# Optimization experiments

Measured on AMD Instinct MI355X. Metric: run time of the kernel, lower is better.

Reference implementation:

```python
import jax, jax.numpy as jnp
import numpy as np
from jax import lax

# Module constraint: hidden_dim == state_dim == expand_dim (see broadcasting in original).
H = 128  # hidden_dim
N = 128  # state_dim
E = 128  # expand_dim = hidden_dim * expand_factor (expand_factor=1)
B, L = 4, 1024


def setup_inputs() -> dict:
    key = jax.random.key(0)
    ks = jax.random.split(key, 11)
    s = lambda fan: 1.0 / np.sqrt(fan)
    return {
        "u": jax.random.normal(ks[0], (B, L, H), jnp.float32),
        "W_in": jax.random.normal(ks[1], (H, 2 * E), jnp.float32) * s(H),
        "b_in": jax.random.normal(ks[2], (2 * E,), jnp.float32) * 0.01,
        "conv_w": jax.random.normal(ks[3], (E, 1, 3), jnp.float32) * s(3),
        "conv_b": jax.random.normal(ks[4], (E,), jnp.float32) * 0.01,
        "W_x": jax.random.normal(ks[5], (E, N + N + H), jnp.float32) * s(E),
        "b_x": jax.random.normal(ks[6], (N + N + H,), jnp.float32) * 0.01,
        "A_log": jax.random.normal(ks[7], (N,), jnp.float32),
        "D": jnp.ones((H,), jnp.float32),
        "W_out": jax.random.normal(ks[8], (E, H), jnp.float32) * s(E),
        "b_out": jax.random.normal(ks[9], (H,), jnp.float32) * 0.01,
    }


def reference(u, W_in, b_in, conv_w, conv_b, W_x, b_x, A_log, D, W_out, b_out):
    b, l, _ = u.shape
    xz = u @ W_in + b_in                       # [B,L,2E]
    x, z = jnp.split(xz, 2, axis=-1)           # [B,L,E] each
    # depthwise conv1d, kernel 3, padding 1 (groups == channels)
    xc = lax.conv_general_dilated(
        x.transpose(0, 2, 1), conv_w, window_strides=(1,), padding=[(1, 1)],
        feature_group_count=E, dimension_numbers=("NCH", "OIH", "NCH"))
    x = jax.nn.silu(xc.transpose(0, 2, 1) + conv_b)  # [B,L,E]
    ssm = x @ W_x + b_x                        # [B,L,2N+H]
    delta = jax.nn.softplus(ssm[..., :N])      # [B,L,N]
    Bm = ssm[..., N:2 * N]                     # [B,L,N]
    C = ssm[..., 2 * N:]                       # [B,L,H]
    A = -jnp.exp(A_log)                        # [N]

    def step(h, inp):
        d_t, B_t, C_t, x_t, u_t = inp          # [B,N],[B,N],[B,H],[B,E],[B,H]
        # A_discrete[b,t,i,j] = exp(delta[b,t,i] * A[j])  (outer broadcast, as in source)
        A_disc = jnp.exp(d_t[:, :, None] * A[None, None, :])       # [B,N,N]
        h = A_disc * h + (d_t * B_t)[:, :, None] * x_t[:, None, :]  # [B,N,E]
        y = (h * C_t[:, None, :]).sum(axis=1) + D * u_t             # [B,H]
        return h, y

    h0 = jnp.zeros((b, N, H), u.dtype)
    inputs = (delta.transpose(1, 0, 2), Bm.transpose(1, 0, 2),
              C.transpose(1, 0, 2), x.transpose(1, 0, 2), u.transpose(1, 0, 2))
    _, ys = lax.scan(step, h0, inputs)         # ys: [L,B,H]
    y = ys.transpose(1, 0, 2) * jax.nn.silu(z)  # [B,L,H] (E==H)
    return y @ W_out + b_out                   # dropout in eval mode: identity
```

## Files before the change

kernel.cpp:

```cpp
#include <hip/hip_runtime.h>
#include <hip/hip_bf16.h>

using bf16 = __hip_bfloat16;
typedef __attribute__((ext_vector_type(8))) short short8;
typedef __attribute__((ext_vector_type(4))) float f32x4;

#define BVAL 4
#define LVAL 1024
#define LOG2E 1.44269504f

#define TSEG 64
#define SSEG 16
#define RSTR 144

#define OFF_U      0
#define OFF_WIN    524288
#define OFF_BIN    557056
#define OFF_CONVW  557312
#define OFF_CONVB  557696
#define OFF_WX     557824
#define OFF_BX     606976
#define OFF_ALOG   607360
#define OFF_D      607488
#define OFF_WOUT   607616
#define OFF_BOUT   624000
#define CVT_TOTAL  624128

#define CVT2_U   524288
#define CVT2_WI  (CVT2_U + 32768)
#define CVT2_WX  (CVT2_WI + 49152)
#define CVT2_TOT (CVT2_WX + 16384)

__device__ __forceinline__ int dtype_flag(const void* D) {
    return ((*(const unsigned int*)D) & 0xFFFFu) != 0u ? 1 : 0;
}
__device__ __forceinline__ float ldin(const void* p, int i, int f) {
    return f ? __bfloat162float(((const bf16*)p)[i]) : ((const float*)p)[i];
}

__global__ void kcvt_all(const void* __restrict__ u, const void* __restrict__ W_in,
                         const void* __restrict__ b_in, const void* __restrict__ conv_w,
                         const void* __restrict__ conv_b, const void* __restrict__ W_x,
                         const void* __restrict__ b_x, const void* __restrict__ A_log,
                         const void* __restrict__ D, const void* __restrict__ W_out,
                         const void* __restrict__ b_out, float* __restrict__ dst,
                         bf16* __restrict__ ubf, bf16* __restrict__ wtin,
                         bf16* __restrict__ wtx, bf16* __restrict__ wtout) {
    int idx = blockIdx.x * 256 + threadIdx.x;
    int f = dtype_flag(D);
    if (idx < CVT_TOTAL) {
        const void* p; int loc;
        if      (idx < OFF_WIN)   { p = u;      loc = idx; }
        else if (idx < OFF_BIN)   { p = W_in;   loc = idx - OFF_WIN; }
        else if (idx < OFF_CONVW) { p = b_in;   loc = idx - OFF_BIN; }
        else if (idx < OFF_CONVB) { p = conv_w; loc = idx - OFF_CONVW; }
        else if (idx < OFF_WX)    { p = conv_b; loc = idx - OFF_CONVB; }
        else if (idx < OFF_BX)    { p = W_x;    loc = idx - OFF_WX; }
        else if (idx < OFF_ALOG)  { p = b_x;    loc = idx - OFF_BX; }
        else if (idx < OFF_D)     { p = A_log;  loc = idx - OFF_ALOG; }
        else if (idx < OFF_WOUT)  { p = D;      loc = idx - OFF_D; }
        else if (idx < OFF_BOUT)  { p = W_out;  loc = idx - OFF_WOUT; }
        else                      { p = b_out;  loc = idx - OFF_BOUT; }
        dst[idx] = ldin(p, loc, f);
    } else {
        int ix = idx - CVT_TOTAL;
        if (ix >= CVT2_TOT) return;
        if (ix < CVT2_U) {
            ubf[ix] = __float2bfloat16(ldin(u, ix, f));
        } else if (ix < CVT2_WI) {
            int rel = ix - CVT2_U; int n = rel >> 7, k = rel & 127;
            wtin[rel] = __float2bfloat16(ldin(W_in, k * 256 + n, f));
        } else if (ix < CVT2_WX) {
            int rel = ix - CVT2_WI; int n = rel >> 7, k = rel & 127;
            wtx[rel] = __float2bfloat16(ldin(W_x, k * 384 + n, f));
        } else {
            int rel = ix - CVT2_WX; int n = rel >> 7, k = rel & 127;
            wtout[rel] = __float2bfloat16(ldin(W_out, k * 128 + n, f));
        }
    }
}

__global__ void k1_mfma(const bf16* __restrict__ ubf, const bf16* __restrict__ wtin,
                        const float* __restrict__ cvt,
                        float* __restrict__ x_pre, float* __restrict__ zs) {
    int blk = blockIdx.x, mb = blk >> 3, cb = blk & 7;
    int tid = threadIdx.x, w = tid >> 6, lane = tid & 63;
    int quad = lane >> 4, sub = lane & 15;
    int m0 = mb * 64 + w * 16, c = cb * 16;
    f32x4 accX = {0.f, 0.f, 0.f, 0.f}, accZ = {0.f, 0.f, 0.f, 0.f};
    #pragma unroll
    for (int ks = 0; ks < 4; ++ks) {
        int k0 = ks * 32 + quad * 8;
        short8 a  = *(const short8*)(ubf + (size_t)(m0 + sub) * 128 + k0);
        short8 bX = *(const short8*)(wtin + (size_t)(c + sub) * 128 + k0);
        short8 bZ = *(const short8*)(wtin + (size_t)(128 + c + sub) * 128 + k0);
        accX = __builtin_amdgcn_mfma_f32_16x16x32_bf16(a, bX, accX, 0, 0, 0);
        accZ = __builtin_amdgcn_mfma_f32_16x16x32_bf16(a, bZ, accZ, 0, 0, 0);
    }
    int o = c + sub;
    float bx_ = cvt[OFF_BIN + o], bz_ = cvt[OFF_BIN + 128 + o];
    #pragma unroll
    for (int r = 0; r < 4; ++r) {
        int m = m0 + quad * 4 + r;
        float x = accX[r] + bx_;
        float z = accZ[r] + bz_;
        x_pre[(size_t)m * 128 + o] = x;
        zs[(size_t)m * 128 + o] = z / (1.0f + __expf(-z));
    }
}

__global__ void k2_conv(const float* __restrict__ cvt, const float* __restrict__ x_pre,
                        float* __restrict__ xs, bf16* __restrict__ xsbf) {
    const float* conv_w = cvt + OFF_CONVW;
    const float* conv_b = cvt + OFF_CONVB;
    int q = blockIdx.x * 256 + threadIdx.x;
    int basee = q * 4;
    int row = basee >> 7;
    int l = row & (LVAL - 1);
    int e = basee & 127;
    float4 xc = *(const float4*)(x_pre + basee);
    float4 xm = make_float4(0.f, 0.f, 0.f, 0.f);
    float4 xp = make_float4(0.f, 0.f, 0.f, 0.f);
    if (l > 0)        xm = *(const float4*)(x_pre + basee - 128);
    if (l < LVAL - 1) xp = *(const float4*)(x_pre + basee + 128);
    float mm[4] = {xm.x, xm.y, xm.z, xm.w};
    float cc[4] = {xc.x, xc.y, xc.z, xc.w};
    float pp[4] = {xp.x, xp.y, xp.z, xp.w};
    float out[4];
    #pragma unroll
    for (int i = 0; i < 4; ++i) {
        float w0 = conv_w[(e + i) * 3 + 0];
        float w1 = conv_w[(e + i) * 3 + 1];
        float w2 = conv_w[(e + i) * 3 + 2];
        float v = fmaf(w0, mm[i], fmaf(w1, cc[i], fmaf(w2, pp[i], conv_b[e + i])));
        out[i] = v / (1.0f + __expf(-v));
    }
    *(float4*)(xs + basee) = make_float4(out[0], out[1], out[2], out[3]);
    #pragma unroll
    for (int i = 0; i < 4; ++i) xsbf[basee + i] = __float2bfloat16(out[i]);
}

__global__ void k3_mfma(const bf16* __restrict__ xsbf, const bf16* __restrict__ wtx,
                        const float* __restrict__ cvt,
                        float* __restrict__ delta, float* __restrict__ dB,
                        float* __restrict__ Cc) {
    int blk = blockIdx.x, mb = blk >> 3, cb = blk & 7;
    int tid = threadIdx.x, w = tid >> 6, lane = tid & 63;
    int quad = lane >> 4, sub = lane & 15;
    int m0 = mb * 64 + w * 16, c = cb * 16;
    f32x4 accA = {0.f,0.f,0.f,0.f}, accB = {0.f,0.f,0.f,0.f}, accC = {0.f,0.f,0.f,0.f};
    #pragma unroll
    for (int ks = 0; ks < 4; ++ks) {
        int k0 = ks * 32 + quad * 8;
        short8 a  = *(const short8*)(xsbf + (size_t)(m0 + sub) * 128 + k0);
        short8 bA = *(const short8*)(wtx + (size_t)(c + sub) * 128 + k0);
        short8 bB = *(const short8*)(wtx + (size_t)(128 + c + sub) * 128 + k0);
        short8 bC = *(const short8*)(wtx + (size_t)(256 + c + sub) * 128 + k0);
        accA = __builtin_amdgcn_mfma_f32_16x16x32_bf16(a, bA, accA, 0, 0, 0);
        accB = __builtin_amdgcn_mfma_f32_16x16x32_bf16(a, bB, accB, 0, 0, 0);
        accC = __builtin_amdgcn_mfma_f32_16x16x32_bf16(a, bC, accC, 0, 0, 0);
    }
    int o = c + sub;
    float ba = cvt[OFF_BX + o], bb = cvt[OFF_BX + 128 + o], bc = cvt[OFF_BX + 256 + o];
    #pragma unroll
    for (int r = 0; r < 4; ++r) {
        int m = m0 + quad * 4 + r;
        size_t idx = (size_t)m * 128 + o;
        float d = accA[r] + ba;
        float sp = (d > 20.0f) ? d : log1pf(__expf(d));
        delta[idx] = sp;
        dB[idx] = sp * (accB[r] + bb);
        Cc[idx] = accC[r] + bc;
    }
}

__device__ __forceinline__ void stage_chunk(float* sdl, float* swl, int tid,
                                            const float4 rd[2], const float4 rw[2]) {
    #pragma unroll
    for (int i = 0; i < 2; ++i) {
        int q = i * 256 + tid;
        int t = q >> 5, n4 = q & 31, l = n4 >> 1, hf = n4 & 1;
        int ad = t * RSTR + 8 * l + 4 * (l >> 2) + 4 * hf;
        *(float4*)&sdl[ad] = rd[i];
        *(float4*)&swl[ad] = rw[i];
    }
}

__global__ __launch_bounds__(256, 2)
void k5a(const float* __restrict__ cvt, const float* __restrict__ delta,
         const float* __restrict__ dB, const float* __restrict__ xs,
         float* __restrict__ hout, float* __restrict__ Pout) {
    __shared__ float sdl[2][16 * RSTR], swl[2][16 * RSTR];
    __shared__ float sx[TSEG][16];
    int blk = blockIdx.x;
    int b = blk >> 7, s = (blk >> 3) & 15, jg = blk & 7;
    int tid = threadIdx.x, w = tid >> 6, lane = tid & 63;
    int cj = lane >> 4, ln = lane & 15;
    int jj = w * 4 + cj, j = jg * 16 + jj;
    int t0 = s * TSEG;
    size_t base = (size_t)b * (LVAL * 128);
    {
        int t = tid >> 2, jc = tid & 3;
        *(float4*)&sx[t][jc * 4] =
            *(const float4*)(xs + base + (size_t)(t0 + t) * 128 + jg * 16 + jc * 4);
    }
    float a2 = -__expf(cvt[OFF_ALOG + j]) * LOG2E;
    const float4* gd4 = (const float4*)(delta + base);
    const float4* gw4 = (const float4*)(dB + base);
    float h[8], p[8];
    #pragma unroll
    for (int i = 0; i < 8; ++i) { h[i] = 0.f; p[i] = 1.f; }
    int fb = t0 * 32;
    float4 rd[2], rw[2];
    rd[0] = gd4[fb + tid]; rd[1] = gd4[fb + 256 + tid];
    rw[0] = gw4[fb + tid]; rw[1] = gw4[fb + 256 + tid];
    stage_chunk(sdl[0], swl[0], tid, rd, rw);
    __syncthreads();
    for (int c4 = 0; c4 < 4; ++c4) {
        if (c4 < 3) {
            int f2 = fb + (c4 + 1) * 512;
            rd[0] = gd4[f2 + tid]; rd[1] = gd4[f2 + 256 + tid];
            rw[0] = gw4[f2 + tid]; rw[1] = gw4[f2 + 256 + tid];
        }
        int bf = c4 & 1;
        int rbase = 8 * ln + 4 * (ln >> 2);
        #pragma unroll 4
        for (int k = 0; k < 16; ++k) {
            int bl = k * RSTR + rbase;
            float4 d0 = *(const float4*)&sdl[bf][bl];
            float4 d1 = *(const float4*)&sdl[bf][bl + 4];
            float4 w0 = *(const float4*)&swl[bf][bl];
            float4 w1 = *(const float4*)&swl[bf][bl + 4];
            float xv = sx[c4 * 16 + k][jj];
            float e;
            e = exp2f(d0.x * a2); h[0] = fmaf(e, h[0], w0.x * xv); p[0] *= e;
            e = exp2f(d0.y * a2); h[1] = fmaf(e, h[1], w0.y * xv); p[1] *= e;
            e = exp2f(d0.z * a2); h[2] = fmaf(e, h[2], w0.z * xv); p[2] *= e;
            e = exp2f(d0.w * a2); h[3] = fmaf(e, h[3], w0.w * xv); p[3] *= e;
            e = exp2f(d1.x * a2); h[4] = fmaf(e, h[4], w1.x * xv); p[4] *= e;
            e = exp2f(d1.y * a2); h[5] = fmaf(e, h[5], w1.y * xv); p[5] *= e;
            e = exp2f(d1.z * a2); h[6] = fmaf(e, h[6], w1.z * xv); p[6] *= e;
            e = exp2f(d1.w * a2); h[7] = fmaf(e, h[7], w1.w * xv); p[7] *= e;
        }
        if (c4 < 3) stage_chunk(sdl[(c4 + 1) & 1], swl[(c4 + 1) & 1], tid, rd, rw);
        __syncthreads();
    }
    size_t cb = (((size_t)(b * SSEG + s) * 128 + j) * 128) + 8 * ln;
    *(float4*)(hout + cb)     = make_float4(h[0], h[1], h[2], h[3]);
    *(float4*)(hout + cb + 4) = make_float4(h[4], h[5], h[6], h[7]);
    *(float4*)(Pout + cb)     = make_float4(p[0], p[1], p[2], p[3]);
    *(float4*)(Pout + cb + 4) = make_float4(p[4], p[5], p[6], p[7]);
}

__global__ __launch_bounds__(256, 2)
void k5c(const float* __restrict__ cvt, const float* __restrict__ delta,
         const float* __restrict__ dB, const float* __restrict__ Cc,
         const float* __restrict__ xs, const float* __restrict__ zs,
         const float* __restrict__ hout, const float* __restrict__ Pout,
         bf16* __restrict__ y2bf) {
    __shared__ float sdl[2][16 * RSTR], swl[2][16 * RSTR];
    __shared__ float sx[TSEG][16], sc[TSEG][16], su[TSEG][16], sz[TSEG][16];
    int blk = blockIdx.x;
    int b = blk >> 7, s = (blk >> 3) & 15, jg = blk & 7;
    int tid = threadIdx.x, w = tid >> 6, lane = tid & 63;
    int cj = lane >> 4, ln = lane & 15;
    int jj = w * 4 + cj, j = jg * 16 + jj;
    int t0 = s * TSEG;
    size_t base = (size_t)b * (LVAL * 128);
    {
        int t = tid >> 2, jc = tid & 3;
        size_t g = base + (size_t)(t0 + t) * 128 + jg * 16 + jc * 4;
        *(float4*)&sx[t][jc * 4] = *(const float4*)(xs + g);
        *(float4*)&sc[t][jc * 4] = *(const float4*)(Cc + g);
        *(float4*)&su[t][jc * 4] = *(const float4*)(cvt + OFF_U + g);
        *(float4*)&sz[t][jc * 4] = *(const float4*)(zs + g);
    }
    float a2 = -__expf(cvt[OFF_ALOG + j]) * LOG2E;
    float Dj = cvt[OFF_D + j];
    const float4* gd4 = (const float4*)(delta + base);
    const float4* gw4 = (const float4*)(dB + base);
    int fb = t0 * 32;
    float4 rd[2], rw[2];
    rd[0] = gd4[fb + tid]; rd[1] = gd4[fb + 256 + tid];
    rw[0] = gw4[fb + tid]; rw[1] = gw4[fb + 256 + tid];
    float h[8];
    #pragma unroll
    for (int i = 0; i < 8; ++i) h[i] = 0.f;
    size_t cstep = (size_t)128 * 128;
    size_t cb0 = (((size_t)(b * SSEG) * 128 + j) * 128) + 8 * ln;
    for (int sp = 0; sp < s; ++sp) {
        size_t cb = cb0 + (size_t)sp * cstep;
        float4 ho0 = *(const float4*)(hout + cb);
        float4 ho1 = *(const float4*)(hout + cb + 4);
        float4 pp0 = *(const float4*)(Pout + cb);
        float4 pp1 = *(const float4*)(Pout + cb + 4);
        h[0] = fmaf(pp0.x, h[0], ho0.x); h[1] = fmaf(pp0.y, h[1], ho0.y);
        h[2] = fmaf(pp0.z, h[2], ho0.z); h[3] = fmaf(pp0.w, h[3], ho0.w);
        h[4] = fmaf(pp1.x, h[4], ho1.x); h[5] = fmaf(pp1.y, h[5], ho1.y);
        h[6] = fmaf(pp1.z, h[6], ho1.z); h[7] = fmaf(pp1.w, h[7], ho1.w);
    }
    stage_chunk(sdl[0], swl[0], tid, rd, rw);
    __syncthreads();
    for (int c4 = 0; c4 < 4; ++c4) {
        if (c4 < 3) {
            int f2 = fb + (c4 + 1) * 512;
            rd[0] = gd4[f2 + tid]; rd[1] = gd4[f2 + 256 + tid];
            rw[0] = gw4[f2 + tid]; rw[1] = gw4[f2 + 256 + tid];
        }
        int bf = c4 & 1;
        int rbase = 8 * ln + 4 * (ln >> 2);
        #pragma unroll 4
        for (int k = 0; k < 16; ++k) {
            int bl = k * RSTR + rbase;
            float4 d0 = *(const float4*)&sdl[bf][bl];
            float4 d1 = *(const float4*)&sdl[bf][bl + 4];
            float4 w0 = *(const float4*)&swl[bf][bl];
            float4 w1 = *(const float4*)&swl[bf][bl + 4];
            int t = c4 * 16 + k;
            float xv = sx[t][jj];
            float e;
            e = exp2f(d0.x * a2); h[0] = fmaf(e, h[0], w0.x * xv);
            e = exp2f(d0.y * a2); h[1] = fmaf(e, h[1], w0.y * xv);
            e = exp2f(d0.z * a2); h[2] = fmaf(e, h[2], w0.z * xv);
            e = exp2f(d0.w * a2); h[3] = fmaf(e, h[3], w0.w * xv);
            e = exp2f(d1.x * a2); h[4] = fmaf(e, h[4], w1.x * xv);
            e = exp2f(d1.y * a2); h[5] = fmaf(e, h[5], w1.y * xv);
            e = exp2f(d1.z * a2); h[6] = fmaf(e, h[6], w1.z * xv);
            e = exp2f(d1.w * a2); h[7] = fmaf(e, h[7], w1.w * xv);
            float sm = ((h[0] + h[1]) + (h[2] + h[3])) + ((h[4] + h[5]) + (h[6] + h[7]));
            sm += __shfl_xor(sm, 1, 64);
            sm += __shfl_xor(sm, 2, 64);
            sm += __shfl_xor(sm, 4, 64);
            sm += __shfl_xor(sm, 8, 64);
            if (ln == 0) {
                float y = fmaf(sc[t][jj], sm, Dj * su[t][jj]);
                y2bf[base + (size_t)(t0 + t) * 128 + j] = __float2bfloat16(y * sz[t][jj]);
            }
        }
        if (c4 < 3) stage_chunk(sdl[(c4 + 1) & 1], swl[(c4 + 1) & 1], tid, rd, rw);
        __syncthreads();
    }
}

__global__ void k6_mfma(const bf16* __restrict__ y2bf, const bf16* __restrict__ wtout,
                        const float* __restrict__ cvt, const void* __restrict__ Din,
                        void* __restrict__ out) {
    int blk = blockIdx.x, mb = blk >> 2, nb = blk & 3;
    int tid = threadIdx.x, w = tid >> 6, lane = tid & 63;
    int quad = lane >> 4, sub = lane & 15;
    int m0 = mb * 64 + w * 16, n0 = nb * 32;
    f32x4 acc0 = {0.f,0.f,0.f,0.f}, acc1 = {0.f,0.f,0.f,0.f};
    #pragma unroll
    for (int ks = 0; ks < 4; ++ks) {
        int k0 = ks * 32 + quad * 8;
        short8 a  = *(const short8*)(y2bf + (size_t)(m0 + sub) * 128 + k0);
        short8 b0 = *(const short8*)(wtout + (size_t)(n0 + sub) * 128 + k0);
        short8 b1 = *(const short8*)(wtout + (size_t)(n0 + 16 + sub) * 128 + k0);
        acc0 = __builtin_amdgcn_mfma_f32_16x16x32_bf16(a, b0, acc0, 0, 0, 0);
        acc1 = __builtin_amdgcn_mfma_f32_16x16x32_bf16(a, b1, acc1, 0, 0, 0);
    }
    int f = dtype_flag(Din);
    float bo0 = cvt[OFF_BOUT + n0 + sub], bo1 = cvt[OFF_BOUT + n0 + 16 + sub];
    #pragma unroll
    for (int r = 0; r < 4; ++r) {
        int m = m0 + quad * 4 + r;
        float v0 = acc0[r] + bo0, v1 = acc1[r] + bo1;
        if (f) {
            ((bf16*)out)[(size_t)m * 128 + n0 + sub] = __float2bfloat16(v0);
            ((bf16*)out)[(size_t)m * 128 + n0 + 16 + sub] = __float2bfloat16(v1);
        } else {
            ((float*)out)[(size_t)m * 128 + n0 + sub] = v0;
            ((float*)out)[(size_t)m * 128 + n0 + 16 + sub] = v1;
        }
    }
}

extern "C" void kernel_launch(void* const* d_in, const int* in_sizes, int n_in,
                              void* d_out, int out_size, void* d_ws, size_t ws_size,
                              hipStream_t stream) {
    const size_t NE = (size_t)BVAL * LVAL * 128;
    const size_t NC = (size_t)BVAL * SSEG * 128 * 128;

    float* cvt   = (float*)d_ws;
    float* bufs  = cvt + CVT_TOTAL;
    float* x_pre = bufs + 0 * NE;
    float* zs    = bufs + 1 * NE;
    float* xs    = bufs + 2 * NE;
    float* delta = bufs + 3 * NE;
    float* dB    = bufs + 4 * NE;
    float* Cc    = bufs + 5 * NE;
    float* hout  = bufs + 6 * NE;
    float* Pou   = hout + NC;
    float* bfarea = Pou + NC;
    bf16* ubf   = (bf16*)bfarea;
    bf16* xsbf  = ubf + NE;
    bf16* y2bf  = xsbf + NE;
    bf16* wtin  = y2bf + NE;
    bf16* wtx   = wtin + 32768;
    bf16* wtout = wtx + 49152;

    const int ROWS = BVAL * LVAL;
    const int CVT_ALL = CVT_TOTAL + CVT2_TOT;

    kcvt_all<<<(CVT_ALL + 255) / 256, 256, 0, stream>>>(
        d_in[0], d_in[1], d_in[2], d_in[3], d_in[4], d_in[5],
        d_in[6], d_in[7], d_in[8], d_in[9], d_in[10],
        cvt, ubf, wtin, wtx, wtout);
    k1_mfma<<<512, 256, 0, stream>>>(ubf, wtin, cvt, x_pre, zs);
    k2_conv<<<(ROWS * 128) / (256 * 4), 256, 0, stream>>>(cvt, x_pre, xs, xsbf);
    k3_mfma<<<512, 256, 0, stream>>>(xsbf, wtx, cvt, delta, dB, Cc);
    k5a<<<BVAL * SSEG * 8, 256, 0, stream>>>(cvt, delta, dB, xs, hout, Pou);
    k5c<<<BVAL * SSEG * 8, 256, 0, stream>>>(cvt, delta, dB, Cc, xs, zs, hout, Pou, y2bf);
    k6_mfma<<<256, 256, 0, stream>>>(y2bf, wtout, cvt, d_in[8], d_out);
}
```

Baseline: 158.1 us.

## Split scan blocks finer over channels and drop redundant fp32 conversions

```diff
diff --git a/kernel.cpp b/kernel.cpp
--- a/kernel.cpp
+++ b/kernel.cpp
@@ -11,7 +11,8 @@
 
 #define TSEG 64
 #define SSEG 16
-#define RSTR 144
+#define CH   16
+#define RST  132
 
 #define OFF_U      0
 #define OFF_WIN    524288
@@ -25,6 +26,7 @@
 #define OFF_WOUT   607616
 #define OFF_BOUT   624000
 #define CVT_TOTAL  624128
+#define FP32N      (CVT_TOTAL - OFF_WIN)
 
 #define CVT2_U   524288
 #define CVT2_WI  (CVT2_U + 32768)
@@ -34,7 +36,7 @@
 __device__ __forceinline__ int dtype_flag(const void* D) {
     return ((*(const unsigned int*)D) & 0xFFFFu) != 0u ? 1 : 0;
 }
-__device__ __forceinline__ float ldin(const void* p, int i, int f) {
+__device__ __forceinline__ float ldin(const void* p, size_t i, int f) {
     return f ? __bfloat162float(((const bf16*)p)[i]) : ((const float*)p)[i];
 }
 
@@ -46,12 +48,12 @@
                          const void* __restrict__ b_out, float* __restrict__ dst,
                          bf16* __restrict__ ubf, bf16* __restrict__ wtin,
                          bf16* __restrict__ wtx, bf16* __restrict__ wtout) {
-    int idx = blockIdx.x * 256 + threadIdx.x;
+    int gidx = blockIdx.x * 256 + threadIdx.x;
     int f = dtype_flag(D);
-    if (idx < CVT_TOTAL) {
+    if (gidx < FP32N) {
+        int idx = gidx + OFF_WIN;
         const void* p; int loc;
-        if      (idx < OFF_WIN)   { p = u;      loc = idx; }
-        else if (idx < OFF_BIN)   { p = W_in;   loc = idx - OFF_WIN; }
+        if      (idx < OFF_BIN)   { p = W_in;   loc = idx - OFF_WIN; }
         else if (idx < OFF_CONVW) { p = b_in;   loc = idx - OFF_BIN; }
         else if (idx < OFF_CONVB) { p = conv_w; loc = idx - OFF_CONVW; }
         else if (idx < OFF_WX)    { p = conv_b; loc = idx - OFF_CONVB; }
@@ -63,7 +65,7 @@
         else                      { p = b_out;  loc = idx - OFF_BOUT; }
         dst[idx] = ldin(p, loc, f);
     } else {
-        int ix = idx - CVT_TOTAL;
+        int ix = gidx - FP32N;
         if (ix >= CVT2_TOT) return;
         if (ix < CVT2_U) {
             ubf[ix] = __float2bfloat16(ldin(u, ix, f));
@@ -82,7 +84,7 @@
 
 __global__ void k1_mfma(const bf16* __restrict__ ubf, const bf16* __restrict__ wtin,
                         const float* __restrict__ cvt,
-                        float* __restrict__ x_pre, float* __restrict__ zs) {
+                        float* __restrict__ x_pre, bf16* __restrict__ zsbf) {
     int blk = blockIdx.x, mb = blk >> 3, cb = blk & 7;
     int tid = threadIdx.x, w = tid >> 6, lane = tid & 63;
     int quad = lane >> 4, sub = lane & 15;
@@ -105,7 +107,7 @@
         float x = accX[r] + bx_;
         float z = accZ[r] + bz_;
         x_pre[(size_t)m * 128 + o] = x;
-        zs[(size_t)m * 128 + o] = z / (1.0f + __expf(-z));
+        zsbf[(size_t)m * 128 + o] = __float2bfloat16(z / (1.0f + __expf(-z)));
     }
 }
 
@@ -174,106 +176,99 @@
     }
 }
 
-__device__ __forceinline__ void stage_chunk(float* sdl, float* swl, int tid,
-                                            const float4 rd[2], const float4 rw[2]) {
-    #pragma unroll
-    for (int i = 0; i < 2; ++i) {
-        int q = i * 256 + tid;
-        int t = q >> 5, n4 = q & 31, l = n4 >> 1, hf = n4 & 1;
-        int ad = t * RSTR + 8 * l + 4 * (l >> 2) + 4 * hf;
-        *(float4*)&sdl[ad] = rd[i];
-        *(float4*)&swl[ad] = rw[i];
-    }
-}
-
-__global__ __launch_bounds__(256, 2)
+
+__global__ __launch_bounds__(256, 4)
 void k5a(const float* __restrict__ cvt, const float* __restrict__ delta,
          const float* __restrict__ dB, const float* __restrict__ xs,
          float* __restrict__ hout, float* __restrict__ Pout) {
-    __shared__ float sdl[2][16 * RSTR], swl[2][16 * RSTR];
-    __shared__ float sx[TSEG][16];
+    __shared__ float sdl[CH * RST], swl[CH * RST];
+    __shared__ float sx[TSEG][8];
     int blk = blockIdx.x;
-    int b = blk >> 7, s = (blk >> 3) & 15, jg = blk & 7;
+    int b = blk >> 8, s = (blk >> 4) & 15, jg = blk & 15;
     int tid = threadIdx.x, w = tid >> 6, lane = tid & 63;
-    int cj = lane >> 4, ln = lane & 15;
-    int jj = w * 4 + cj, j = jg * 16 + jj;
+    int cj = lane >> 5, ln = lane & 31;
+    int jj = w * 2 + cj, j = jg * 8 + jj;
     int t0 = s * TSEG;
     size_t base = (size_t)b * (LVAL * 128);
     {
-        int t = tid >> 2, jc = tid & 3;
-        *(float4*)&sx[t][jc * 4] =
-            *(const float4*)(xs + base + (size_t)(t0 + t) * 128 + jg * 16 + jc * 4);
+        #pragma unroll
+        for (int i = 0; i < 2; ++i) {
+            int q = i * 256 + tid;
+            int t = q >> 3, jc = q & 7;
+            sx[t][jc] = xs[base + (size_t)(t0 + t) * 128 + jg * 8 + jc];
+        }
     }
     float a2 = -__expf(cvt[OFF_ALOG + j]) * LOG2E;
     const float4* gd4 = (const float4*)(delta + base);
     const float4* gw4 = (const float4*)(dB + base);
-    float h[8], p[8];
-    #pragma unroll
-    for (int i = 0; i < 8; ++i) { h[i] = 0.f; p[i] = 1.f; }
     int fb = t0 * 32;
     float4 rd[2], rw[2];
     rd[0] = gd4[fb + tid]; rd[1] = gd4[fb + 256 + tid];
     rw[0] = gw4[fb + tid]; rw[1] = gw4[fb + 256 + tid];
-    stage_chunk(sdl[0], swl[0], tid, rd, rw);
-    __syncthreads();
+    float h[4] = {0.f, 0.f, 0.f, 0.f};
+    float p[4] = {1.f, 1.f, 1.f, 1.f};
     for (int c4 = 0; c4 < 4; ++c4) {
+        #pragma unroll
+        for (int i = 0; i < 2; ++i) {
+            int q = i * 256 + tid;
+            int t = q >> 5, c4i = q & 31;
+            *(float4*)&sdl[t * RST + 4 * c4i] = rd[i];
+            *(float4*)&swl[t * RST + 4 * c4i] = rw[i];
+        }
+        __syncthreads();
         if (c4 < 3) {
             int f2 = fb + (c4 + 1) * 512;
             rd[0] = gd4[f2 + tid]; rd[1] = gd4[f2 + 256 + tid];
             rw[0] = gw4[f2 + tid]; rw[1] = gw4[f2 + 256 + tid];
         }
-        int bf = c4 & 1;
-        int rbase = 8 * ln + 4 * (ln >> 2);
         #pragma unroll 4
-        for (int k = 0; k < 16; ++k) {
-            int bl = k * RSTR + rbase;
-            float4 d0 = *(const float4*)&sdl[bf][bl];
-            float4 d1 = *(const float4*)&sdl[bf][bl + 4];
-            float4 w0 = *(const float4*)&swl[bf][bl];
-            float4 w1 = *(const float4*)&swl[bf][bl + 4];
-            float xv = sx[c4 * 16 + k][jj];
+        for (int k = 0; k < CH; ++k) {
+            int bl = k * RST + 4 * ln;
+            float4 d = *(const float4*)&sdl[bl];
+            float4 wv = *(const float4*)&swl[bl];
+            float xv = sx[c4 * CH + k][jj];
             float e;
-            e = exp2f(d0.x * a2); h[0] = fmaf(e, h[0], w0.x * xv); p[0] *= e;
-            e = exp2f(d0.y * a2); h[1] = fmaf(e, h[1], w0.y * xv); p[1] *= e;
-            e = exp2f(d0.z * a2); h[2] = fmaf(e, h[2], w0.z * xv); p[2] *= e;
-            e = exp2f(d0.w * a2); h[3] = fmaf(e, h[3], w0.w * xv); p[3] *= e;
-            e = exp2f(d1.x * a2); h[4] = fmaf(e, h[4], w1.x * xv); p[4] *= e;
-            e = exp2f(d1.y * a2); h[5] = fmaf(e, h[5], w1.y * xv); p[5] *= e;
-            e = exp2f(d1.z * a2); h[6] = fmaf(e, h[6], w1.z * xv); p[6] *= e;
-            e = exp2f(d1.w * a2); h[7] = fmaf(e, h[7], w1.w * xv); p[7] *= e;
-        }
-        if (c4 < 3) stage_chunk(sdl[(c4 + 1) & 1], swl[(c4 + 1) & 1], tid, rd, rw);
+            e = exp2f(d.x * a2); h[0] = fmaf(e, h[0], wv.x * xv); p[0] *= e;
+            e = exp2f(d.y * a2); h[1] = fmaf(e, h[1], wv.y * xv); p[1] *= e;
+            e = exp2f(d.z * a2); h[2] = fmaf(e, h[2], wv.z * xv); p[2] *= e;
+            e = exp2f(d.w * a2); h[3] = fmaf(e, h[3], wv.w * xv); p[3] *= e;
+        }
         __syncthreads();
     }
-    size_t cb = (((size_t)(b * SSEG + s) * 128 + j) * 128) + 8 * ln;
-    *(float4*)(hout + cb)     = make_float4(h[0], h[1], h[2], h[3]);
-    *(float4*)(hout + cb + 4) = make_float4(h[4], h[5], h[6], h[7]);
-    *(float4*)(Pout + cb)     = make_float4(p[0], p[1], p[2], p[3]);
-    *(float4*)(Pout + cb + 4) = make_float4(p[4], p[5], p[6], p[7]);
-}
-
-__global__ __launch_bounds__(256, 2)
+    size_t cb = (((size_t)(b * SSEG + s) * 128 + j) * 128) + 4 * ln;
+    *(float4*)(hout + cb) = make_float4(h[0], h[1], h[2], h[3]);
+    *(float4*)(Pout + cb) = make_float4(p[0], p[1], p[2], p[3]);
+}
+
+__global__ __launch_bounds__(256, 4)
 void k5c(const float* __restrict__ cvt, const float* __restrict__ delta,
          const float* __restrict__ dB, const float* __restrict__ Cc,
-         const float* __restrict__ xs, const float* __restrict__ zs,
+         const float* __restrict__ xs, const bf16* __restrict__ zsbf,
+         const void* __restrict__ uin, const void* __restrict__ Din,
          const float* __restrict__ hout, const float* __restrict__ Pout,
          bf16* __restrict__ y2bf) {
-    __shared__ float sdl[2][16 * RSTR], swl[2][16 * RSTR];
-    __shared__ float sx[TSEG][16], sc[TSEG][16], su[TSEG][16], sz[TSEG][16];
+    __shared__ float sdl[CH * RST], swl[CH * RST];
+    __shared__ float sx[TSEG][8], sc[TSEG][8], su[TSEG][8], sz[TSEG][8];
+    __shared__ float sy[TSEG][8];
     int blk = blockIdx.x;
-    int b = blk >> 7, s = (blk >> 3) & 15, jg = blk & 7;
+    int b = blk >> 8, s = (blk >> 4) & 15, jg = blk & 15;
     int tid = threadIdx.x, w = tid >> 6, lane = tid & 63;
-    int cj = lane >> 4, ln = lane & 15;
-    int jj = w * 4 + cj, j = jg * 16 + jj;
+    int cj = lane >> 5, ln = lane & 31;
+    int jj = w * 2 + cj, j = jg * 8 + jj;
     int t0 = s * TSEG;
+    int f = dtype_flag(Din);
     size_t base = (size_t)b * (LVAL * 128);
     {
-        int t = tid >> 2, jc = tid & 3;
-        size_t g = base + (size_t)(t0 + t) * 128 + jg * 16 + jc * 4;
-        *(float4*)&sx[t][jc * 4] = *(const float4*)(xs + g);
-        *(float4*)&sc[t][jc * 4] = *(const float4*)(Cc + g);
-        *(float4*)&su[t][jc * 4] = *(const float4*)(cvt + OFF_U + g);
-        *(float4*)&sz[t][jc * 4] = *(const float4*)(zs + g);
+        #pragma unroll
+        for (int i = 0; i < 2; ++i) {
+            int q = i * 256 + tid;
+            int t = q >> 3, jc = q & 7;
+            size_t g = base + (size_t)(t0 + t) * 128 + jg * 8 + jc;
+            sx[t][jc] = xs[g];
+            sc[t][jc] = Cc[g];
+            su[t][jc] = ldin(uin, g, f);
+            sz[t][jc] = __bfloat162float(zsbf[g]);
+        }
     }
     float a2 = -__expf(cvt[OFF_ALOG + j]) * LOG2E;
     float Dj = cvt[OFF_D + j];
@@ -283,62 +278,60 @@
     float4 rd[2], rw[2];
     rd[0] = gd4[fb + tid]; rd[1] = gd4[fb + 256 + tid];
     rw[0] = gw4[fb + tid]; rw[1] = gw4[fb + 256 + tid];
-    float h[8];
-    #pragma unroll
-    for (int i = 0; i < 8; ++i) h[i] = 0.f;
+    float h[4] = {0.f, 0.f, 0.f, 0.f};
     size_t cstep = (size_t)128 * 128;
-    size_t cb0 = (((size_t)(b * SSEG) * 128 + j) * 128) + 8 * ln;
+    size_t cb0 = (((size_t)(b * SSEG) * 128 + j) * 128) + 4 * ln;
     for (int sp = 0; sp < s; ++sp) {
         size_t cb = cb0 + (size_t)sp * cstep;
-        float4 ho0 = *(const float4*)(hout + cb);
-        float4 ho1 = *(const float4*)(hout + cb + 4);
-        float4 pp0 = *(const float4*)(Pout + cb);
-        float4 pp1 = *(const float4*)(Pout + cb + 4);
-        h[0] = fmaf(pp0.x, h[0], ho0.x); h[1] = fmaf(pp0.y, h[1], ho0.y);
-        h[2] = fmaf(pp0.z, h[2], ho0.z); h[3] = fmaf(pp0.w, h[3], ho0.w);
-        h[4] = fmaf(pp1.x, h[4], ho1.x); h[5] = fmaf(pp1.y, h[5], ho1.y);
-        h[6] = fmaf(pp1.z, h[6], ho1.z); h[7] = fmaf(pp1.w, h[7], ho1.w);
-    }
-    stage_chunk(sdl[0], swl[0], tid, rd, rw);
-    __syncthreads();
+        float4 ho = *(const float4*)(hout + cb);
+        float4 pp = *(const float4*)(Pout + cb);
+        h[0] = fmaf(pp.x, h[0], ho.x); h[1] = fmaf(pp.y, h[1], ho.y);
+        h[2] = fmaf(pp.z, h[2], ho.z); h[3] = fmaf(pp.w, h[3], ho.w);
+    }
     for (int c4 = 0; c4 < 4; ++c4) {
+        #pragma unroll
+        for (int i = 0; i < 2; ++i) {
+            int q = i * 256 + tid;
+            int t = q >> 5, c4i = q & 31;
+            *(float4*)&sdl[t * RST + 4 * c4i] = rd[i];
+            *(float4*)&swl[t * RST + 4 * c4i] = rw[i];
+        }
+        __syncthreads();
         if (c4 < 3) {
             int f2 = fb + (c4 + 1) * 512;
             rd[0] = gd4[f2 + tid]; rd[1] = gd4[f2 + 256 + tid];
             rw[0] = gw4[f2 + tid]; rw[1] = gw4[f2 + 256 + tid];
         }
-        int bf = c4 & 1;
-        int rbase = 8 * ln + 4 * (ln >> 2);
         #pragma unroll 4
-        for (int k = 0; k < 16; ++k) {
-            int bl = k * RSTR + rbase;
-            float4 d0 = *(const float4*)&sdl[bf][bl];
-            float4 d1 = *(const float4*)&sdl[bf][bl + 4];
-            float4 w0 = *(const float4*)&swl[bf][bl];
-            float4 w1 = *(const float4*)&swl[bf][bl + 4];
-            int t = c4 * 16 + k;
+        for (int k = 0; k < CH; ++k) {
+            int bl = k * RST + 4 * ln;
+            float4 d = *(const float4*)&sdl[bl];
+            float4 wv = *(const float4*)&swl[bl];
+            int t = c4 * CH + k;
             float xv = sx[t][jj];
             float e;
-            e = exp2f(d0.x * a2); h[0] = fmaf(e, h[0], w0.x * xv);
-            e = exp2f(d0.y * a2); h[1] = fmaf(e, h[1], w0.y * xv);
-            e = exp2f(d0.z * a2); h[2] = fmaf(e, h[2], w0.z * xv);
-            e = exp2f(d0.w * a2); h[3] = fmaf(e, h[3], w0.w * xv);
-            e = exp2f(d1.x * a2); h[4] = fmaf(e, h[4], w1.x * xv);
-            e = exp2f(d1.y * a2); h[5] = fmaf(e, h[5], w1.y * xv);
-            e = exp2f(d1.z * a2); h[6] = fmaf(e, h[6], w1.z * xv);
-            e = exp2f(d1.w * a2); h[7] = fmaf(e, h[7], w1.w * xv);
-            float sm = ((h[0] + h[1]) + (h[2] + h[3])) + ((h[4] + h[5]) + (h[6] + h[7]));
+            e = exp2f(d.x * a2); h[0] = fmaf(e, h[0], wv.x * xv);
+            e = exp2f(d.y * a2); h[1] = fmaf(e, h[1], wv.y * xv);
+            e = exp2f(d.z * a2); h[2] = fmaf(e, h[2], wv.z * xv);
+            e = exp2f(d.w * a2); h[3] = fmaf(e, h[3], wv.w * xv);
+            float sm = (h[0] + h[1]) + (h[2] + h[3]);
             sm += __shfl_xor(sm, 1, 64);
             sm += __shfl_xor(sm, 2, 64);
             sm += __shfl_xor(sm, 4, 64);
             sm += __shfl_xor(sm, 8, 64);
+            sm += __shfl_xor(sm, 16, 64);
             if (ln == 0) {
                 float y = fmaf(sc[t][jj], sm, Dj * su[t][jj]);
-                y2bf[base + (size_t)(t0 + t) * 128 + j] = __float2bfloat16(y * sz[t][jj]);
+                sy[t][jj] = y * sz[t][jj];
             }
         }
-        if (c4 < 3) stage_chunk(sdl[(c4 + 1) & 1], swl[(c4 + 1) & 1], tid, rd, rw);
         __syncthreads();
+    }
+    #pragma unroll
+    for (int i = 0; i < 2; ++i) {
+        int q = i * 256 + tid;
+        int t = q >> 3, jc = q & 7;
+        y2bf[base + (size_t)(t0 + t) * 128 + jg * 8 + jc] = __float2bfloat16(sy[t][jc]);
     }
 }
 
@@ -384,7 +377,7 @@
     float* cvt   = (float*)d_ws;
     float* bufs  = cvt + CVT_TOTAL;
     float* x_pre = bufs + 0 * NE;
-    float* zs    = bufs + 1 * NE;
+    float* zsb   = bufs + 1 * NE;
     float* xs    = bufs + 2 * NE;
     float* delta = bufs + 3 * NE;
     float* dB    = bufs + 4 * NE;
@@ -392,6 +385,7 @@
     float* hout  = bufs + 6 * NE;
     float* Pou   = hout + NC;
     float* bfarea = Pou + NC;
+    bf16* zsbf  = (bf16*)zsb;
     bf16* ubf   = (bf16*)bfarea;
     bf16* xsbf  = ubf + NE;
     bf16* y2bf  = xsbf + NE;
@@ -400,16 +394,17 @@
     bf16* wtout = wtx + 49152;
 
     const int ROWS = BVAL * LVAL;
-    const int CVT_ALL = CVT_TOTAL + CVT2_TOT;
+    const int CVT_ALL = FP32N + CVT2_TOT;
 
     kcvt_all<<<(CVT_ALL + 255) / 256, 256, 0, stream>>>(
         d_in[0], d_in[1], d_in[2], d_in[3], d_in[4], d_in[5],
         d_in[6], d_in[7], d_in[8], d_in[9], d_in[10],
         cvt, ubf, wtin, wtx, wtout);
-    k1_mfma<<<512, 256, 0, stream>>>(ubf, wtin, cvt, x_pre, zs);
+    k1_mfma<<<512, 256, 0, stream>>>(ubf, wtin, cvt, x_pre, zsbf);
     k2_conv<<<(ROWS * 128) / (256 * 4), 256, 0, stream>>>(cvt, x_pre, xs, xsbf);
     k3_mfma<<<512, 256, 0, stream>>>(xsbf, wtx, cvt, delta, dB, Cc);
-    k5a<<<BVAL * SSEG * 8, 256, 0, stream>>>(cvt, delta, dB, xs, hout, Pou);
-    k5c<<<BVAL * SSEG * 8, 256, 0, stream>>>(cvt, delta, dB, Cc, xs, zs, hout, Pou, y2bf);
+    k5a<<<BVAL * SSEG * 16, 256, 0, stream>>>(cvt, delta, dB, xs, hout, Pou);
+    k5c<<<BVAL * SSEG * 16, 256, 0, stream>>>(cvt, delta, dB, Cc, xs, zsbf,
+                                              d_in[0], d_in[8], hout, Pou, y2bf);
     k6_mfma<<<256, 256, 0, stream>>>(y2bf, wtout, cvt, d_in[8], d_out);
 }
```

Result: slower. 171.5 us (+8.5%).
